# Optimization experiments

Measured on AMD Instinct MI355X. Metric: run time of the kernel, lower is better.

Reference implementation:

```python
import jax, jax.numpy as jnp
import numpy as np

LN_EPS = 1e-5

def _layernorm(x, g, b):
    mu = jnp.mean(x, axis=-1, keepdims=True)
    var = jnp.var(x, axis=-1, keepdims=True)
    return (x - mu) * jax.lax.rsqrt(var + LN_EPS) * g + b

def _attention(q_in, ctx, wq, wk, wv, wo, bo, n_heads):
    b, n, _ = q_in.shape
    m = ctx.shape[1]
    d_attn = wq.shape[1]
    d_head = d_attn // n_heads
    Q = (q_in @ wq).reshape(b, n, n_heads, d_head)
    K = (ctx @ wk).reshape(b, m, n_heads, d_head)
    V = (ctx @ wv).reshape(b, m, n_heads, d_head)
    scale = 1.0 / np.sqrt(d_head).astype(np.float32)
    sim = jnp.einsum('bnhd,bmhd->bhnm', Q, K) * scale
    attn = jax.nn.softmax(sim, axis=-1)
    out = jnp.einsum('bhnm,bmhd->bnhd', attn, V).reshape(b, n, d_attn)
    return out @ wo + bo

def setup_inputs() -> dict:
    key = jax.random.key(0)
    ks = jax.random.split(key, 16)
    B, N, D = 8, 1024, 640
    M, CD = 77, 768
    H = 4 * D  # GEGLU hidden = 2560
    s = lambda d: 1.0 / np.sqrt(d)
    return {
        'x': jax.random.normal(ks[0], (B, N, D), jnp.float32),
        'context': jax.random.normal(ks[1], (B, M, CD), jnp.float32),
        'sa_wq': jax.random.normal(ks[2], (D, D), jnp.float32) * s(D),
        'sa_wk': jax.random.normal(ks[3], (D, D), jnp.float32) * s(D),
        'sa_wv': jax.random.normal(ks[4], (D, D), jnp.float32) * s(D),
        'sa_wo': jax.random.normal(ks[5], (D, D), jnp.float32) * s(D),
        'sa_bo': jnp.zeros((D,), jnp.float32),
        'ca_wq': jax.random.normal(ks[6], (D, D), jnp.float32) * s(D),
        'ca_wk': jax.random.normal(ks[7], (CD, D), jnp.float32) * s(CD),
        'ca_wv': jax.random.normal(ks[8], (CD, D), jnp.float32) * s(CD),
        'ca_wo': jax.random.normal(ks[9], (D, D), jnp.float32) * s(D),
        'ca_bo': jnp.zeros((D,), jnp.float32),
        'ff_w1': jax.random.normal(ks[10], (D, 2 * H), jnp.float32) * s(D),
        'ff_b1': jnp.zeros((2 * H,), jnp.float32),
        'ff_w2': jax.random.normal(ks[11], (H, D), jnp.float32) * s(H),
        'ff_b2': jnp.zeros((D,), jnp.float32),
        'ln1_g': jnp.ones((D,), jnp.float32), 'ln1_b': jnp.zeros((D,), jnp.float32),
        'ln2_g': jnp.ones((D,), jnp.float32), 'ln2_b': jnp.zeros((D,), jnp.float32),
        'ln3_g': jnp.ones((D,), jnp.float32), 'ln3_b': jnp.zeros((D,), jnp.float32),
    }

def reference(x, context, sa_wq, sa_wk, sa_wv, sa_wo, sa_bo,
              ca_wq, ca_wk, ca_wv, ca_wo, ca_bo,
              ff_w1, ff_b1, ff_w2, ff_b2,
              ln1_g, ln1_b, ln2_g, ln2_b, ln3_g, ln3_b):
    n_heads = 8
    # post-norm residual block, matching norm_i(x + sublayer(x))
    x = _layernorm(x + _attention(x, x, sa_wq, sa_wk, sa_wv, sa_wo, sa_bo, n_heads), ln1_g, ln1_b)
    x = _layernorm(x + _attention(x, context, ca_wq, ca_wk, ca_wv, ca_wo, ca_bo, n_heads), ln2_g, ln2_b)
    h = x @ ff_w1 + ff_b1
    a, gate = jnp.split(h, 2, axis=-1)
    ff = (a * jax.nn.gelu(gate, approximate=False)) @ ff_w2 + ff_b2
    x = _layernorm(x + ff, ln3_g, ln3_b)
    return x
```

## Files before the change

### kernel.cpp

```cpp
#include <hip/hip_runtime.h>


using u16 = unsigned short;
typedef __attribute__((ext_vector_type(8))) short bfrag;
typedef __attribute__((ext_vector_type(4))) float f4;
typedef __attribute__((ext_vector_type(4))) unsigned short us4;

#define MFMA(a, b, c) __builtin_amdgcn_mfma_f32_16x16x32_bf16((a), (b), (c), 0, 0, 0)

__device__ __forceinline__ void gload16(const void* g, void* l) {
    __builtin_amdgcn_global_load_lds(
        (const __attribute__((address_space(1))) void*)g,
        (__attribute__((address_space(3))) void*)l, 16, 0, 0);
}

__device__ __forceinline__ u16 f2b(float f) {
    unsigned u = __float_as_uint(f);
    unsigned r = u + 0x7FFFu + ((u >> 16) & 1u);
    return (u16)(r >> 16);
}
__device__ __forceinline__ float b2f(u16 u) {
    return __uint_as_float(((unsigned)u) << 16);
}
__device__ __forceinline__ unsigned pack2(float a, float b) {
    return (unsigned)f2b(a) | ((unsigned)f2b(b) << 16);
}
__device__ __forceinline__ bfrag bzero() {
    bfrag z = {0,0,0,0,0,0,0,0};
    return z;
}
__device__ __forceinline__ float gelu_f(float x) {
    float y = 0.7978845608028654f * (x + 0.044715f * x * x * x);
    float e = exp2f(y * 2.8853900817779268f);
    float t = 1.0f - 2.0f * __builtin_amdgcn_rcpf(e + 1.0f);
    return 0.5f * x * (1.0f + t);
}

__device__ __forceinline__ void transp_tile(const float* __restrict__ in,
                                            u16* __restrict__ out,
                                            int K, int N, int ldo,
                                            int tile, bool perm,
                                            float (*t)[33])
{
    int nw = N >> 5;
    int n0 = (tile % nw) * 32, k0 = (tile / nw) * 32;
    int tx = threadIdx.x & 31, ty = threadIdx.x >> 5;
    #pragma unroll
    for (int i = 0; i < 32; i += 8)
        t[ty + i][tx] = in[(size_t)(k0 + ty + i) * N + n0 + tx];
    __syncthreads();
    #pragma unroll
    for (int i = 0; i < 32; i += 8) {
        int n = n0 + ty + i;
        int dst;
        if (perm) {
            dst = (n < 2560) ? ((n >> 5) * 64 + (n & 31))
                             : (((n - 2560) >> 5) * 64 + 32 + ((n - 2560) & 31));
        } else {
            dst = n;
        }
        out[(size_t)dst * ldo + k0 + tx] = f2b(t[tx][ty + i]);
    }
}

__global__ __launch_bounds__(256) void prep_k(
    const float* __restrict__ x, const float* __restrict__ ctx,
    const float* __restrict__ sa_wq, const float* __restrict__ sa_wk,
    const float* __restrict__ sa_wv, const float* __restrict__ sa_wo,
    const float* __restrict__ ca_wq, const float* __restrict__ ca_wk,
    const float* __restrict__ ca_wv, const float* __restrict__ ca_wo,
    const float* __restrict__ ff_w1, const float* __restrict__ ff_w2,
    u16* saqkvt, u16* sawot, u16* cawqt, u16* cawot, u16* cakvt,
    u16* ffw1t, u16* ffw2t, u16* xb, u16* ctxb)
{
    __shared__ float t[32][33];
    int b = blockIdx.x;
    if (b < 2400) {
        int task = b / 400, tile = b - task * 400;
        const float* src;
        u16* dst;
        if      (task == 0) { src = sa_wq; dst = saqkvt; }
        else if (task == 1) { src = sa_wk; dst = saqkvt + 409600; }
        else if (task == 2) { src = sa_wv; dst = saqkvt + 819200; }
        else if (task == 3) { src = sa_wo; dst = sawot; }
        else if (task == 4) { src = ca_wq; dst = cawqt; }
        else                { src = ca_wo; dst = cawot; }
        transp_tile(src, dst, 640, 640, 640, tile, false, t);
    } else if (b < 3360) {
        int tt = b - 2400;
        int task = tt / 480, tile = tt - task * 480;
        transp_tile(task ? ca_wv : ca_wk, cakvt + task * 491520, 768, 640, 768,
                    tile, false, t);
    } else if (b < 6560) {
        transp_tile(ff_w1, ffw1t, 640, 5120, 640, b - 3360, true, t);
    } else if (b < 8160) {
        transp_tile(ff_w2, ffw2t, 2560, 640, 2560, b - 6560, false, t);
    } else if (b < 10720) {
        int i = (b - 8160) * 256 + threadIdx.x;
        const float4* p = (const float4*)x + (size_t)i * 2;
        float4 a = p[0], bb = p[1];
        uint4 w = { pack2(a.x, a.y), pack2(a.z, a.w),
                    pack2(bb.x, bb.y), pack2(bb.z, bb.w) };
        ((uint4*)xb)[i] = w;
    } else {
        int i = (b - 10720) * 256 + threadIdx.x;
        int rowOut = i / 96, c8 = (i - rowOut * 96) * 8;
        int bb = rowOut / 80, r = rowOut - bb * 80;
        uint4 w = {0, 0, 0, 0};
        if (r < 77) {
            const float4* p = (const float4*)(ctx + ((size_t)(bb * 77 + r)) * 768 + c8);
            float4 a = p[0], b2 = p[1];
            w = (uint4){ pack2(a.x, a.y), pack2(a.z, a.w),
                         pack2(b2.x, b2.y), pack2(b2.z, b2.w) };
        }
        ((uint4*)ctxb)[i] = w;
    }
}

template<int MODE>
__device__ __forceinline__ void gemm_core(const u16* __restrict__ A,
                                          const u16* __restrict__ Bt,
                                          int N, int K,
                                          const float* __restrict__ bias,
                                          const u16* __restrict__ resb,
                                          float* __restrict__ outf,
                                          u16* __restrict__ outb,
                                          u16* __restrict__ out2,
                                          int bx, int by,
                                          u16* As, u16* Bs)
{
    const int lane = threadIdx.x & 63;
    const int wid  = threadIdx.x >> 6;
    const int q    = lane >> 4;
    const int lc   = lane & 15;
    const int wm = wid >> 1, wn = wid & 1;
    const int m0 = by * 128;
    const int n0 = bx * 128;

    f4 acc[4][4];
    #pragma unroll
    for (int i = 0; i < 4; ++i)
        #pragma unroll
        for (int j = 0; j < 4; ++j) acc[i][j] = (f4){0.f, 0.f, 0.f, 0.f};

    const char* Abase = (const char*)A + (size_t)m0 * (size_t)(K * 2);
    const char* Bbase = (const char*)Bt + (size_t)n0 * (size_t)(K * 2);

    for (int kt = 0; kt < K; kt += 64) {
        #pragma unroll
        for (int c = 0; c < 4; ++c) {
            int cid = wid * 4 + c;
            int o = cid * 1024 + lane * 16;
            int row = o >> 7;
            int pc  = o & 127;
            int src = pc ^ ((row & 7) << 4);
            gload16(Abase + (size_t)row * (K * 2) + kt * 2 + src, (char*)As + cid * 1024);
            gload16(Bbase + (size_t)row * (K * 2) + kt * 2 + src, (char*)Bs + cid * 1024);
        }
        __syncthreads();
        #pragma unroll
        for (int ks = 0; ks < 2; ++ks) {
            bfrag a[4], b[4];
            #pragma unroll
            for (int mi = 0; mi < 4; ++mi) {
                int row = wm * 64 + mi * 16 + lc;
                int off = row * 128 + ((ks * 64 + q * 16) ^ ((row & 7) << 4));
                a[mi] = *(const bfrag*)((const char*)As + off);
            }
            #pragma unroll
            for (int ni = 0; ni < 4; ++ni) {
                int row = wn * 64 + ni * 16 + lc;
                int off = row * 128 + ((ks * 64 + q * 16) ^ ((row & 7) << 4));
                b[ni] = *(const bfrag*)((const char*)Bs + off);
            }
            #pragma unroll
            for (int mi = 0; mi < 4; ++mi)
                #pragma unroll
                for (int ni = 0; ni < 4; ++ni)
                    acc[mi][ni] = MFMA(a[mi], b[ni], acc[mi][ni]);
        }
        __syncthreads();
    }

    const int baseRow = m0 + wm * 64;
    const int baseCol = n0 + wn * 64;

    if (MODE == 4) {
        const int blk = baseCol >> 6;
        #pragma unroll
        for (int mi = 0; mi < 4; ++mi)
            #pragma unroll
            for (int ni = 0; ni < 2; ++ni) {
                int j = blk * 32 + ni * 16 + lc;
                float ba = bias[j];
                float bg = bias[2560 + j];
                #pragma unroll
                for (int r = 0; r < 4; ++r) {
                    int row = baseRow + mi * 16 + q * 4 + r;
                    float aa = acc[mi][ni][r] + ba;
                    float gg = acc[mi][ni + 2][r] + bg;
                    outb[(size_t)row * 2560 + j] = f2b(aa * gelu_f(gg));
                }
            }
        return;
    }

    #pragma unroll
    for (int mi = 0; mi < 4; ++mi)
        #pragma unroll
        for (int ni = 0; ni < 4; ++ni) {
            int col = baseCol + ni * 16 + lc;
            if (MODE == 2) {
                us4 vv = {0, 0, 0, 0};
                #pragma unroll
                for (int r = 0; r < 4; ++r) {
                    int row = baseRow + mi * 16 + q * 4 + r;
                    u16 u = f2b(acc[mi][ni][r]);
                    outb[(size_t)row * 1920 + col] = u;
                    vv[r] = u;
                }
                if (col >= 1280) {
                    int cd = col - 1280;
                    int hh = cd / 80, dd = cd - hh * 80;
                    int row0 = baseRow + mi * 16 + q * 4;
                    int bb = row0 >> 10, tok = row0 & 1023;
                    *(us4*)&out2[(size_t)((bb * 8 + hh) * 80 + dd) * 1024 + tok] = vv;
                }
            } else {
                #pragma unroll
                for (int r = 0; r < 4; ++r) {
                    int row = baseRow + mi * 16 + q * 4 + r;
                    float v = acc[mi][ni][r];
                    if (MODE == 0) {
                        v += bias[col] + b2f(resb[(size_t)row * N + col]);
                        outf[(size_t)row * N + col] = v;
                    } else if (MODE == 1) {
                        outb[(size_t)row * N + col] = f2b(v);
                    } else if (MODE == 3) {
                        int bb = row / 80, rr = row - bb * 80;
                        if (rr < 77) {
                            u16 u = f2b(v);
                            if (col < 640) {
                                outb[(size_t)row * 640 + col] = u;
                            } else {
                                int cd = col - 640;
                                int hh = cd / 80, dd = cd - hh * 80;
                                out2[((bb * 8 + hh) * 80 + dd) * 80 + rr] = u;
                            }
                        }
                    }
                }
            }
        }
}

template<int MODE>
__global__ __launch_bounds__(256) void gemm_bt(const u16* __restrict__ A,
                                               const u16* __restrict__ Bt,
                                               int N, int K,
                                               const float* __restrict__ bias,
                                               const u16* __restrict__ resb,
                                               float* __restrict__ outf,
                                               u16* __restrict__ outb,
                                               u16* __restrict__ out2)
{
    __shared__ u16 As[128 * 64];
    __shared__ u16 Bs[128 * 64];
    gemm_core<MODE>(A, Bt, N, K, bias, resb, outf, outb, out2,
                    blockIdx.x, blockIdx.y, As, Bs);
}

__global__ __launch_bounds__(256) void gemm_qkv_cakv(
    const u16* __restrict__ xb, const u16* __restrict__ saqkvt,
    const u16* __restrict__ ctxb, const u16* __restrict__ cakvt,
    u16* qkvb, u16* vt, u16* kc, u16* vct)
{
    __shared__ u16 As[128 * 64];
    __shared__ u16 Bs[128 * 64];
    int bid = blockIdx.x;
    if (bid < 960) {
        gemm_core<2>(xb, saqkvt, 1920, 640, nullptr, nullptr, nullptr,
                     qkvb, vt, bid % 15, bid / 15, As, Bs);
    } else {
        int tt = bid - 960;
        gemm_core<3>(ctxb, cakvt, 1280, 768, nullptr, nullptr, nullptr,
                     kc, vct, tt % 10, tt / 10, As, Bs);
    }
}

__global__ __launch_bounds__(256) void attn_sa(const u16* __restrict__ qkv,
                                               const u16* __restrict__ vt,
                                               u16* __restrict__ out)
{
    __shared__ u16 Qs[64 * 80];
    __shared__ u16 Ks[64 * 80];
    __shared__ u16 Vs[80 * 64];
    __shared__ u16 Ps[4][16 * 64];

    const int lane = threadIdx.x & 63;
    const int wid  = threadIdx.x >> 6;
    const int q    = lane >> 4;
    const int lc   = lane & 15;
    const int bid = blockIdx.x;
    const int qt = bid & 15;
    const int hh = (bid >> 4) & 7;
    const int bb = bid >> 7;
    const int tok0 = bb * 1024 + qt * 64;
    const char* qbase = (const char*)qkv;

    for (int c = wid; c < 10; c += 4) {
        int o = c * 1024 + lane * 16;
        int row = o / 160, col = o - row * 160;
        gload16(qbase + (size_t)(tok0 + row) * 3840 + hh * 160 + col, (char*)Qs + c * 1024);
    }
    __syncthreads();

    const int qrow = wid * 16 + lc;
    bfrag qf0 = *(const bfrag*)((const char*)Qs + qrow * 160 + q * 16);
    bfrag qf1 = *(const bfrag*)((const char*)Qs + qrow * 160 + 64 + q * 16);
    bfrag qf2 = bzero();
    if (q < 2) qf2 = *(const bfrag*)((const char*)Qs + qrow * 160 + 128 + q * 16);

    float mrow[4], lrow[4];
    f4 accO[5];
    #pragma unroll
    for (int r = 0; r < 4; ++r) { mrow[r] = -3e38f; lrow[r] = 0.f; }
    #pragma unroll
    for (int no = 0; no < 5; ++no) accO[no] = (f4){0.f, 0.f, 0.f, 0.f};

    const float SC = 0.11180339887498949f;
    const float L2E = 1.4426950408889634f;

    for (int t = 0; t < 16; ++t) {
        __syncthreads();
        for (int c = wid; c < 20; c += 4) {
            if (c < 10) {
                int o = c * 1024 + lane * 16;
                int row = o / 160, col = o - row * 160;
                gload16(qbase + (size_t)(bb * 1024 + t * 64 + row) * 3840 + 1280 + hh * 160 + col,
                        (char*)Ks + c * 1024);
            } else {
                int c2 = c - 10;
                int o = c2 * 1024 + lane * 16;
                int row = o >> 7;
                int pc  = o & 127;
                int src = pc ^ ((row & 7) << 4);
                gload16((const char*)vt + (size_t)((bb * 8 + hh) * 80 + row) * 2048 + t * 128 + src,
                        (char*)Vs + c2 * 1024);
            }
        }
        __syncthreads();

        f4 s[4];
        #pragma unroll
        for (int nb = 0; nb < 4; ++nb) {
            const char* kb = (const char*)Ks + (nb * 16 + lc) * 160;
            bfrag k0 = *(const bfrag*)(kb + q * 16);
            bfrag k1 = *(const bfrag*)(kb + 64 + q * 16);
            bfrag k2 = bzero();
            if (q < 2) k2 = *(const bfrag*)(kb + 128 + q * 16);
            f4 a = {0.f, 0.f, 0.f, 0.f};
            a = MFMA(qf0, k0, a);
            a = MFMA(qf1, k1, a);
            a = MFMA(qf2, k2, a);
            s[nb] = a;
        }
        #pragma unroll
        for (int nb = 0; nb < 4; ++nb)
            #pragma unroll
            for (int r = 0; r < 4; ++r) s[nb][r] *= SC;

        float rmax[4], alpha[4];
        #pragma unroll
        for (int r = 0; r < 4; ++r) {
            float v = fmaxf(fmaxf(s[0][r], s[1][r]), fmaxf(s[2][r], s[3][r]));
            v = fmaxf(v, __shfl_xor(v, 1));
            v = fmaxf(v, __shfl_xor(v, 2));
            v = fmaxf(v, __shfl_xor(v, 4));
            v = fmaxf(v, __shfl_xor(v, 8));
            rmax[r] = v;
        }
        #pragma unroll
        for (int r = 0; r < 4; ++r) {
            float mn = fmaxf(mrow[r], rmax[r]);
            alpha[r] = exp2f((mrow[r] - mn) * L2E);
            mrow[r] = mn;
        }
        float rsum[4] = {0.f, 0.f, 0.f, 0.f};
        #pragma unroll
        for (int nb = 0; nb < 4; ++nb)
            #pragma unroll
            for (int r = 0; r < 4; ++r) {
                float p = exp2f((s[nb][r] - mrow[r]) * L2E);
                s[nb][r] = p;
                rsum[r] += p;
            }
        #pragma unroll
        for (int r = 0; r < 4; ++r) {
            float v = rsum[r];
            v += __shfl_xor(v, 1);
            v += __shfl_xor(v, 2);
            v += __shfl_xor(v, 4);
            v += __shfl_xor(v, 8);
            lrow[r] = lrow[r] * alpha[r] + v;
        }
        #pragma unroll
        for (int no = 0; no < 5; ++no)
            #pragma unroll
            for (int r = 0; r < 4; ++r) accO[no][r] *= alpha[r];

        char* Pw = (char*)&Ps[wid][0];
        #pragma unroll
        for (int nb = 0; nb < 4; ++nb)
            #pragma unroll
            for (int r = 0; r < 4; ++r) {
                int prow = q * 4 + r;
                int off = prow * 128 + (((nb * 16 + lc) * 2) ^ ((prow & 7) << 4));
                *(u16*)(Pw + off) = f2b(s[nb][r]);
            }
        bfrag pa0 = *(const bfrag*)(Pw + lc * 128 + ((q * 16) ^ ((lc & 7) << 4)));
        bfrag pa1 = *(const bfrag*)(Pw + lc * 128 + ((64 + q * 16) ^ ((lc & 7) << 4)));
        #pragma unroll
        for (int no = 0; no < 5; ++no) {
            int vr = no * 16 + lc;
            const char* vb = (const char*)Vs + vr * 128;
            bfrag v0 = *(const bfrag*)(vb + ((q * 16) ^ ((vr & 7) << 4)));
            bfrag v1 = *(const bfrag*)(vb + ((64 + q * 16) ^ ((vr & 7) << 4)));
            accO[no] = MFMA(pa0, v0, accO[no]);
            accO[no] = MFMA(pa1, v1, accO[no]);
        }
    }

    #pragma unroll
    for (int no = 0; no < 5; ++no)
        #pragma unroll
        for (int r = 0; r < 4; ++r) {
            int row = tok0 + wid * 16 + q * 4 + r;
            int col = hh * 80 + no * 16 + lc;
            out[(size_t)row * 640 + col] = f2b(accO[no][r] / lrow[r]);
        }
}

__global__ __launch_bounds__(256) void attn_ca(const u16* __restrict__ qc,
                                               const u16* __restrict__ kc,
                                               const u16* __restrict__ vct,
                                               u16* __restrict__ out)
{
    __shared__ u16 Qs[64 * 80];
    __shared__ u16 Ks[84 * 80];
    __shared__ u16 Vs[84 * 80];
    __shared__ u16 Ps[4][16 * 80];

    const int lane = threadIdx.x & 63;
    const int wid  = threadIdx.x >> 6;
    const int q    = lane >> 4;
    const int lc   = lane & 15;
    const int bid = blockIdx.x;
    const int qt = bid & 15;
    const int hh = (bid >> 4) & 7;
    const int bb = bid >> 7;
    const int tok0 = bb * 1024 + qt * 64;

    for (int c = wid; c < 36; c += 4) {
        if (c < 10) {
            int o = c * 1024 + lane * 16;
            int row = o / 160, col = o - row * 160;
            gload16((const char*)qc + (size_t)(tok0 + row) * 1280 + hh * 160 + col,
                    (char*)Qs + c * 1024);
        } else if (c < 23) {
            int c2 = c - 10;
            int o = c2 * 1024 + lane * 16;
            int row = o / 160, col = o - row * 160;
            gload16((const char*)kc + (size_t)(bb * 80 + row) * 1280 + hh * 160 + col,
                    (char*)Ks + c2 * 1024);
        } else {
            int c2 = c - 23;
            int o = c2 * 1024 + lane * 16;
            int row = o / 160, col = o - row * 160;
            gload16((const char*)vct + (size_t)((bb * 8 + hh) * 80 + row) * 160 + col,
                    (char*)Vs + c2 * 1024);
        }
    }
    __syncthreads();

    const int qrow = wid * 16 + lc;
    bfrag qf0 = *(const bfrag*)((const char*)Qs + qrow * 160 + q * 16);
    bfrag qf1 = *(const bfrag*)((const char*)Qs + qrow * 160 + 64 + q * 16);
    bfrag qf2 = bzero();
    if (q < 2) qf2 = *(const bfrag*)((const char*)Qs + qrow * 160 + 128 + q * 16);

    const float SC = 0.11180339887498949f;
    const float L2E = 1.4426950408889634f;

    f4 s[5];
    #pragma unroll
    for (int nb = 0; nb < 5; ++nb) {
        const char* kb = (const char*)Ks + (nb * 16 + lc) * 160;
        bfrag k0 = *(const bfrag*)(kb + q * 16);
        bfrag k1 = *(const bfrag*)(kb + 64 + q * 16);
        bfrag k2 = bzero();
        if (q < 2) k2 = *(const bfrag*)(kb + 128 + q * 16);
        f4 a = {0.f, 0.f, 0.f, 0.f};
        a = MFMA(qf0, k0, a);
        a = MFMA(qf1, k1, a);
        a = MFMA(qf2, k2, a);
        s[nb] = a;
    }
    #pragma unroll
    for (int nb = 0; nb < 5; ++nb) {
        int key = nb * 16 + lc;
        #pragma unroll
        for (int r = 0; r < 4; ++r) {
            s[nb][r] *= SC;
            if (key >= 77) s[nb][r] = -1e30f;
        }
    }
    float mrow[4], lrow[4];
    #pragma unroll
    for (int r = 0; r < 4; ++r) {
        float v = fmaxf(fmaxf(fmaxf(s[0][r], s[1][r]), fmaxf(s[2][r], s[3][r])), s[4][r]);
        v = fmaxf(v, __shfl_xor(v, 1));
        v = fmaxf(v, __shfl_xor(v, 2));
        v = fmaxf(v, __shfl_xor(v, 4));
        v = fmaxf(v, __shfl_xor(v, 8));
        mrow[r] = v;
    }
    float rsum[4] = {0.f, 0.f, 0.f, 0.f};
    #pragma unroll
    for (int nb = 0; nb < 5; ++nb)
        #pragma unroll
        for (int r = 0; r < 4; ++r) {
            float p = exp2f((s[nb][r] - mrow[r]) * L2E);
            s[nb][r] = p;
            rsum[r] += p;
        }
    #pragma unroll
    for (int r = 0; r < 4; ++r) {
        float v = rsum[r];
        v += __shfl_xor(v, 1);
        v += __shfl_xor(v, 2);
        v += __shfl_xor(v, 4);
        v += __shfl_xor(v, 8);
        lrow[r] = v;
    }

    char* Pw = (char*)&Ps[wid][0];
    #pragma unroll
    for (int nb = 0; nb < 5; ++nb)
        #pragma unroll
        for (int r = 0; r < 4; ++r) {
            int prow = q * 4 + r;
            *(u16*)(Pw + prow * 160 + (nb * 16 + lc) * 2) = f2b(s[nb][r]);
        }
    bfrag pa0 = *(const bfrag*)(Pw + lc * 160 + q * 16);
    bfrag pa1 = *(const bfrag*)(Pw + lc * 160 + 64 + q * 16);
    bfrag pa2 = bzero();
    if (q < 2) pa2 = *(const bfrag*)(Pw + lc * 160 + 128 + q * 16);

    f4 accO[5];
    #pragma unroll
    for (int no = 0; no < 5; ++no) {
        const char* vb = (const char*)Vs + (no * 16 + lc) * 160;
        bfrag v0 = *(const bfrag*)(vb + q * 16);
        bfrag v1 = *(const bfrag*)(vb + 64 + q * 16);
        bfrag v2 = bzero();
        if (q < 2) v2 = *(const bfrag*)(vb + 128 + q * 16);
        f4 a = {0.f, 0.f, 0.f, 0.f};
        a = MFMA(pa0, v0, a);
        a = MFMA(pa1, v1, a);
        a = MFMA(pa2, v2, a);
        accO[no] = a;
    }
    #pragma unroll
    for (int no = 0; no < 5; ++no)
        #pragma unroll
        for (int r = 0; r < 4; ++r) {
            int row = tok0 + wid * 16 + q * 4 + r;
            int col = hh * 80 + no * 16 + lc;
            out[(size_t)row * 640 + col] = f2b(accO[no][r] / lrow[r]);
        }
}

__global__ __launch_bounds__(256) void ln_k(const float* __restrict__ pre,
                                            const float* __restrict__ g,
                                            const float* __restrict__ b,
                                            float* __restrict__ xo,
                                            u16* __restrict__ xb)
{
    const int lane = threadIdx.x & 63;
    const int wid  = threadIdx.x >> 6;
    const int row = blockIdx.x * 4 + wid;
    const float* p = pre + (size_t)row * 640;
    float v[10];
    #pragma unroll
    for (int i = 0; i < 10; ++i) v[i] = p[lane + i * 64];
    float s = 0.f;
    #pragma unroll
    for (int i = 0; i < 10; ++i) s += v[i];
    #pragma unroll
    for (int m = 1; m < 64; m <<= 1) s += __shfl_xor(s, m);
    float mu = s * (1.0f / 640.0f);
    float d2 = 0.f;
    #pragma unroll
    for (int i = 0; i < 10; ++i) { float d = v[i] - mu; d2 += d * d; }
    #pragma unroll
    for (int m = 1; m < 64; m <<= 1) d2 += __shfl_xor(d2, m);
    float rs = rsqrtf(d2 * (1.0f / 640.0f) + 1e-5f);
    #pragma unroll
    for (int i = 0; i < 10; ++i) {
        int col = lane + i * 64;
        float y = (v[i] - mu) * rs * g[col] + b[col];
        if (xo) xo[(size_t)row * 640 + col] = y;
        if (xb) xb[(size_t)row * 640 + col] = f2b(y);
    }
}

extern "C" void kernel_launch(void* const* d_in, const int* in_sizes, int n_in,
                              void* d_out, int out_size, void* d_ws, size_t ws_size,
                              hipStream_t stream)
{
    const float* x       = (const float*)d_in[0];
    const float* context = (const float*)d_in[1];
    const float* sa_wq = (const float*)d_in[2];
    const float* sa_wk = (const float*)d_in[3];
    const float* sa_wv = (const float*)d_in[4];
    const float* sa_wo = (const float*)d_in[5];
    const float* sa_bo = (const float*)d_in[6];
    const float* ca_wq = (const float*)d_in[7];
    const float* ca_wk = (const float*)d_in[8];
    const float* ca_wv = (const float*)d_in[9];
    const float* ca_wo = (const float*)d_in[10];
    const float* ca_bo = (const float*)d_in[11];
    const float* ff_w1 = (const float*)d_in[12];
    const float* ff_b1 = (const float*)d_in[13];
    const float* ff_w2 = (const float*)d_in[14];
    const float* ff_b2 = (const float*)d_in[15];
    const float* ln1_g = (const float*)d_in[16];
    const float* ln1_b = (const float*)d_in[17];
    const float* ln2_g = (const float*)d_in[18];
    const float* ln2_b = (const float*)d_in[19];
    const float* ln3_g = (const float*)d_in[20];
    const float* ln3_b = (const float*)d_in[21];

    char* ws = (char*)d_ws;
    const size_t OFF_XB     = 0;
    const size_t OFF_QKVB   = 10485760;
    const size_t OFF_VT     = 41943040;
    const size_t OFF_AB     = 52428800;
    const size_t OFF_ATTN   = 62914560;
    const size_t OFF_QC     = 73400320;
    const size_t OFF_KC     = 83886080;
    const size_t OFF_VCT    = 84705280;
    const size_t OFF_SAQKVT = 85524480;
    const size_t OFF_SAWOT  = 87982080;
    const size_t OFF_CAWQT  = 88801280;
    const size_t OFF_CAKVT  = 89620480;
    const size_t OFF_CAWOT  = 91586560;
    const size_t OFF_FFW1T  = 92405760;
    const size_t OFF_FFW2T  = 98959360;
    const size_t OFF_CTXB   = 102236160;
    const size_t OFF_PRE    = 103219200;

    u16* xb      = (u16*)(ws + OFF_XB);
    u16* qkvb    = (u16*)(ws + OFF_QKVB);
    u16* vt      = (u16*)(ws + OFF_VT);
    u16* ab      = (u16*)(ws + OFF_AB);
    u16* attnb   = (u16*)(ws + OFF_ATTN);
    u16* qc      = (u16*)(ws + OFF_QC);
    u16* kc      = (u16*)(ws + OFF_KC);
    u16* vct     = (u16*)(ws + OFF_VCT);
    u16* saqkvt  = (u16*)(ws + OFF_SAQKVT);
    u16* sawot   = (u16*)(ws + OFF_SAWOT);
    u16* cawqt   = (u16*)(ws + OFF_CAWQT);
    u16* cakvt   = (u16*)(ws + OFF_CAKVT);
    u16* cawot   = (u16*)(ws + OFF_CAWOT);
    u16* ffw1t   = (u16*)(ws + OFF_FFW1T);
    u16* ffw2t   = (u16*)(ws + OFF_FFW2T);
    u16* ctxb    = (u16*)(ws + OFF_CTXB);
    float* pre   = (float*)(ws + OFF_PRE);
    u16* ffh     = (u16*)(ws + OFF_XB);

    hipLaunchKernelGGL(prep_k, dim3(10960), dim3(256), 0, stream,
                       x, context, sa_wq, sa_wk, sa_wv, sa_wo, ca_wq, ca_wk,
                       ca_wv, ca_wo, ff_w1, ff_w2,
                       saqkvt, sawot, cawqt, cawot, cakvt, ffw1t, ffw2t, xb, ctxb);

    hipLaunchKernelGGL(gemm_qkv_cakv, dim3(1010), dim3(256), 0, stream,
                       xb, saqkvt, ctxb, cakvt, qkvb, vt, kc, vct);
    hipLaunchKernelGGL(attn_sa, dim3(1024), dim3(256), 0, stream, qkvb, vt, attnb);
    hipLaunchKernelGGL(gemm_bt<0>, dim3(5, 64), dim3(256), 0, stream,
                       attnb, sawot, 640, 640, sa_bo, xb, pre,
                       (u16*)nullptr, (u16*)nullptr);
    hipLaunchKernelGGL(ln_k, dim3(2048), dim3(256), 0, stream, pre, ln1_g, ln1_b,
                       (float*)nullptr, ab);

    hipLaunchKernelGGL(gemm_bt<1>, dim3(5, 64), dim3(256), 0, stream,
                       ab, cawqt, 640, 640, (const float*)nullptr, (const u16*)nullptr,
                       (float*)nullptr, qc, (u16*)nullptr);
    hipLaunchKernelGGL(attn_ca, dim3(1024), dim3(256), 0, stream, qc, kc, vct, attnb);
    hipLaunchKernelGGL(gemm_bt<0>, dim3(5, 64), dim3(256), 0, stream,
                       attnb, cawot, 640, 640, ca_bo, ab, pre,
                       (u16*)nullptr, (u16*)nullptr);
    hipLaunchKernelGGL(ln_k, dim3(2048), dim3(256), 0, stream, pre, ln2_g, ln2_b,
                       (float*)nullptr, ab);

    hipLaunchKernelGGL(gemm_bt<4>, dim3(40, 64), dim3(256), 0, stream,
                       ab, ffw1t, 5120, 640, ff_b1, (const u16*)nullptr,
                       (float*)nullptr, ffh, (u16*)nullptr);
    hipLaunchKernelGGL(gemm_bt<0>, dim3(5, 64), dim3(256), 0, stream,
                       ffh, ffw2t, 640, 2560, ff_b2, ab, pre,
                       (u16*)nullptr, (u16*)nullptr);
    hipLaunchKernelGGL(ln_k, dim3(2048), dim3(256), 0, stream, pre, ln3_g, ln3_b,
                       (float*)d_out, (u16*)nullptr);
}
```

Before: 373.6 us.

## Transpose self-attention score MFMA, fold softmax scale into Q, lazy rescale

```diff
diff --git a/kernel.cpp b/kernel.cpp
--- a/kernel.cpp
+++ b/kernel.cpp
@@ -211,11 +211,12 @@
         for (int ni = 0; ni < 4; ++ni) {
             int col = baseCol + ni * 16 + lc;
             if (MODE == 2) {
+                const float qs = (col < 640) ? 0.11180339887498949f : 1.0f;
                 us4 vv = {0, 0, 0, 0};
                 #pragma unroll
                 for (int r = 0; r < 4; ++r) {
                     int row = baseRow + mi * 16 + q * 4 + r;
-                    u16 u = f2b(acc[mi][ni][r]);
+                    u16 u = f2b(acc[mi][ni][r] * qs);
                     outb[(size_t)row * 1920 + col] = u;
                     vv[r] = u;
                 }
@@ -299,12 +300,12 @@
 
     const int lane = threadIdx.x & 63;
     const int wid  = threadIdx.x >> 6;
-    const int q    = lane >> 4;
+    const int hi   = lane >> 4;
     const int lc   = lane & 15;
     const int bid = blockIdx.x;
-    const int qt = bid & 15;
-    const int hh = (bid >> 4) & 7;
-    const int bb = bid >> 7;
+    const int qt = bid >> 6;
+    const int bb = (bid >> 3) & 7;
+    const int hh = bid & 7;
     const int tok0 = bb * 1024 + qt * 64;
     const char* qbase = (const char*)qkv;
 
@@ -316,19 +317,16 @@
     __syncthreads();
 
     const int qrow = wid * 16 + lc;
-    bfrag qf0 = *(const bfrag*)((const char*)Qs + qrow * 160 + q * 16);
-    bfrag qf1 = *(const bfrag*)((const char*)Qs + qrow * 160 + 64 + q * 16);
+    bfrag qf0 = *(const bfrag*)((const char*)Qs + qrow * 160 + hi * 16);
+    bfrag qf1 = *(const bfrag*)((const char*)Qs + qrow * 160 + 64 + hi * 16);
     bfrag qf2 = bzero();
-    if (q < 2) qf2 = *(const bfrag*)((const char*)Qs + qrow * 160 + 128 + q * 16);
-
-    float mrow[4], lrow[4];
+    if (hi < 2) qf2 = *(const bfrag*)((const char*)Qs + qrow * 160 + 128 + hi * 16);
+
+    float m = -3e30f, l = 0.f;
     f4 accO[5];
     #pragma unroll
-    for (int r = 0; r < 4; ++r) { mrow[r] = -3e38f; lrow[r] = 0.f; }
-    #pragma unroll
     for (int no = 0; no < 5; ++no) accO[no] = (f4){0.f, 0.f, 0.f, 0.f};
 
-    const float SC = 0.11180339887498949f;
     const float L2E = 1.4426950408889634f;
 
     for (int t = 0; t < 16; ++t) {
@@ -351,93 +349,90 @@
         }
         __syncthreads();
 
-        f4 s[4];
+        f4 sT[4];
         #pragma unroll
         for (int nb = 0; nb < 4; ++nb) {
             const char* kb = (const char*)Ks + (nb * 16 + lc) * 160;
-            bfrag k0 = *(const bfrag*)(kb + q * 16);
-            bfrag k1 = *(const bfrag*)(kb + 64 + q * 16);
+            bfrag k0 = *(const bfrag*)(kb + hi * 16);
+            bfrag k1 = *(const bfrag*)(kb + 64 + hi * 16);
             bfrag k2 = bzero();
-            if (q < 2) k2 = *(const bfrag*)(kb + 128 + q * 16);
+            if (hi < 2) k2 = *(const bfrag*)(kb + 128 + hi * 16);
             f4 a = {0.f, 0.f, 0.f, 0.f};
-            a = MFMA(qf0, k0, a);
-            a = MFMA(qf1, k1, a);
-            a = MFMA(qf2, k2, a);
-            s[nb] = a;
-        }
+            a = MFMA(k0, qf0, a);
+            a = MFMA(k1, qf1, a);
+            a = MFMA(k2, qf2, a);
+            sT[nb] = a;
+        }
+
+        float pm = sT[0][0];
         #pragma unroll
         for (int nb = 0; nb < 4; ++nb)
             #pragma unroll
-            for (int r = 0; r < 4; ++r) s[nb][r] *= SC;
-
-        float rmax[4], alpha[4];
-        #pragma unroll
-        for (int r = 0; r < 4; ++r) {
-            float v = fmaxf(fmaxf(s[0][r], s[1][r]), fmaxf(s[2][r], s[3][r]));
-            v = fmaxf(v, __shfl_xor(v, 1));
-            v = fmaxf(v, __shfl_xor(v, 2));
-            v = fmaxf(v, __shfl_xor(v, 4));
-            v = fmaxf(v, __shfl_xor(v, 8));
-            rmax[r] = v;
-        }
-        #pragma unroll
-        for (int r = 0; r < 4; ++r) {
-            float mn = fmaxf(mrow[r], rmax[r]);
-            alpha[r] = exp2f((mrow[r] - mn) * L2E);
-            mrow[r] = mn;
-        }
-        float rsum[4] = {0.f, 0.f, 0.f, 0.f};
+            for (int r = 0; r < 4; ++r) pm = fmaxf(pm, sT[nb][r]);
+        pm = fmaxf(pm, __shfl_xor(pm, 16));
+        pm = fmaxf(pm, __shfl_xor(pm, 32));
+
+        if (__any(pm > m + 8.0f)) {
+            float mn = fmaxf(m, pm);
+            float al = exp2f((m - mn) * L2E);
+            m = mn;
+            l *= al;
+            float af[4];
+            #pragma unroll
+            for (int r = 0; r < 4; ++r) af[r] = __shfl(al, hi * 4 + r);
+            #pragma unroll
+            for (int no = 0; no < 5; ++no)
+                #pragma unroll
+                for (int r = 0; r < 4; ++r) accO[no][r] *= af[r];
+        }
+
+        float sum = 0.f;
         #pragma unroll
         for (int nb = 0; nb < 4; ++nb)
             #pragma unroll
             for (int r = 0; r < 4; ++r) {
-                float p = exp2f((s[nb][r] - mrow[r]) * L2E);
-                s[nb][r] = p;
-                rsum[r] += p;
+                float p = exp2f((sT[nb][r] - m) * L2E);
+                sT[nb][r] = p;
+                sum += p;
             }
-        #pragma unroll
-        for (int r = 0; r < 4; ++r) {
-            float v = rsum[r];
-            v += __shfl_xor(v, 1);
-            v += __shfl_xor(v, 2);
-            v += __shfl_xor(v, 4);
-            v += __shfl_xor(v, 8);
-            lrow[r] = lrow[r] * alpha[r] + v;
-        }
-        #pragma unroll
-        for (int no = 0; no < 5; ++no)
-            #pragma unroll
-            for (int r = 0; r < 4; ++r) accO[no][r] *= alpha[r];
+        sum += __shfl_xor(sum, 16);
+        sum += __shfl_xor(sum, 32);
+        l += sum;
 
         char* Pw = (char*)&Ps[wid][0];
         #pragma unroll
-        for (int nb = 0; nb < 4; ++nb)
-            #pragma unroll
-            for (int r = 0; r < 4; ++r) {
-                int prow = q * 4 + r;
-                int off = prow * 128 + (((nb * 16 + lc) * 2) ^ ((prow & 7) << 4));
-                *(u16*)(Pw + off) = f2b(s[nb][r]);
-            }
-        bfrag pa0 = *(const bfrag*)(Pw + lc * 128 + ((q * 16) ^ ((lc & 7) << 4)));
-        bfrag pa1 = *(const bfrag*)(Pw + lc * 128 + ((64 + q * 16) ^ ((lc & 7) << 4)));
+        for (int nb = 0; nb < 4; ++nb) {
+            us4 pk = { f2b(sT[nb][0]), f2b(sT[nb][1]), f2b(sT[nb][2]), f2b(sT[nb][3]) };
+            int cb = (nb * 16 + hi * 4) * 2;
+            *(us4*)(Pw + lc * 128 + (cb ^ ((lc & 7) << 4))) = pk;
+        }
+
+        bfrag pa0 = *(const bfrag*)(Pw + lc * 128 + ((hi * 16) ^ ((lc & 7) << 4)));
+        bfrag pa1 = *(const bfrag*)(Pw + lc * 128 + ((64 + hi * 16) ^ ((lc & 7) << 4)));
         #pragma unroll
         for (int no = 0; no < 5; ++no) {
             int vr = no * 16 + lc;
             const char* vb = (const char*)Vs + vr * 128;
-            bfrag v0 = *(const bfrag*)(vb + ((q * 16) ^ ((vr & 7) << 4)));
-            bfrag v1 = *(const bfrag*)(vb + ((64 + q * 16) ^ ((vr & 7) << 4)));
+            bfrag v0 = *(const bfrag*)(vb + ((hi * 16) ^ ((vr & 7) << 4)));
+            bfrag v1 = *(const bfrag*)(vb + ((64 + hi * 16) ^ ((vr & 7) << 4)));
             accO[no] = MFMA(pa0, v0, accO[no]);
             accO[no] = MFMA(pa1, v1, accO[no]);
         }
     }
 
+    float rf[4];
+    #pragma unroll
+    for (int r = 0; r < 4; ++r) {
+        float lf = __shfl(l, hi * 4 + r);
+        rf[r] = __builtin_amdgcn_rcpf(lf);
+    }
     #pragma unroll
     for (int no = 0; no < 5; ++no)
         #pragma unroll
         for (int r = 0; r < 4; ++r) {
-            int row = tok0 + wid * 16 + q * 4 + r;
+            int row = tok0 + wid * 16 + hi * 4 + r;
             int col = hh * 80 + no * 16 + lc;
-            out[(size_t)row * 640 + col] = f2b(accO[no][r] / lrow[r]);
+            out[(size_t)row * 640 + col] = f2b(accO[no][r] * rf[r]);
         }
 }
 
```

After: 355.3 us. 4.9% less time.
